# Optimization experiments

Hardware: AMD Instinct MI355X
Metric: run time of the kernel (lower is better)

Reference implementation:

```python
import jax, jax.numpy as jnp
import numpy as np

B, N, D = 16, 2048, 64

def setup_inputs() -> dict:
    key = jax.random.key(0)
    kq, kk, kv = jax.random.split(key, 3)
    queries = jax.random.normal(kq, (B, N, D), dtype=jnp.float32)
    keys = jax.random.normal(kk, (B, N, D), dtype=jnp.float32)
    values = jax.random.normal(kv, (B, N, D), dtype=jnp.float32)
    scaling_factor = jnp.asarray(np.sqrt(D), dtype=jnp.float32)
    return {"queries": queries, "keys": keys, "values": values, "scaling_factor": scaling_factor}

def reference(queries, keys, values, scaling_factor):
    # scores: [B, N, N] = Q K^T / scale
    scores = jnp.einsum('bqd,bkd->bqk', queries, keys) / scaling_factor
    atn = jax.nn.softmax(scores, axis=2)
    return jnp.einsum('bqk,bkd->bqd', atn, values)
```

## Files before the change

kernel.cpp:

```cpp
#include <hip/hip_runtime.h>
#include <hip/hip_bf16.h>

#define BATCH 16
#define SEQ 2048
#define DIM 64

typedef __attribute__((ext_vector_type(8))) __bf16 bf16x8;
typedef __attribute__((ext_vector_type(8))) unsigned short u16x8;
typedef __attribute__((ext_vector_type(2))) unsigned int u32x2;
typedef __attribute__((ext_vector_type(4))) unsigned int u32x4;
typedef __attribute__((ext_vector_type(16))) float f32x16;

#if __has_builtin(__builtin_amdgcn_exp2f)
#define EXP2F(x) __builtin_amdgcn_exp2f(x)
#else
#define EXP2F(x) __expf(0.69314718055994531f * (x))
#endif

__device__ __forceinline__ unsigned short f2bf_hw(float f) {
    __bf16 h = (__bf16)f;
    return __builtin_bit_cast(unsigned short, h);
}

__device__ __forceinline__ unsigned int pk_bf16(float lo, float hi) {
    unsigned int a = f2bf_hw(lo), b = f2bf_hw(hi);
    return a | (b << 16);
}

__device__ __forceinline__ void half_swap(unsigned int a, unsigned int b,
                                          unsigned int& lo, unsigned int& hi) {
#if __has_builtin(__builtin_amdgcn_permlane32_swap)
    u32x2 r = __builtin_amdgcn_permlane32_swap(a, b, false, false);
    lo = r[0];
    hi = r[1];
#else
    unsigned int sa = (unsigned int)__shfl_xor((int)a, 32);
    unsigned int sb = (unsigned int)__shfl_xor((int)b, 32);
    const bool hh = (threadIdx.x & 32) != 0;
    lo = hh ? sb : a;
    hi = hh ? b : sa;
#endif
}

__global__ __launch_bounds__(256)
void preconvert_kv(const float* __restrict__ K, const float* __restrict__ V,
                   unsigned short* __restrict__ Ks, unsigned short* __restrict__ Vts) {
    __shared__ float vt[128 * 65];
    const int tid = threadIdx.x;
    const int x = blockIdx.x;
    const int b = ((x & 7) << 1) | ((x >> 3) & 1);
    const int kpath = (x >> 4) & 1;
    const int t = x >> 5;
    if (kpath) {
        const float* src = K + ((size_t)(b * SEQ + t * 128)) * DIM;
        unsigned short* dst = Ks + ((size_t)(b * 16 + t)) * 8192;
        #pragma unroll
        for (int p = 0; p < 4; ++p) {
            const int cid = p * 256 + tid;
            const int key = cid >> 3, g = cid & 7;
            const int d0 = (g >> 1) * 16 + (g & 1) * 8;
            float4 x0 = *(const float4*)(src + key * DIM + d0);
            float4 x1 = *(const float4*)(src + key * DIM + d0 + 4);
            u16x8 o;
            o[0] = f2bf_hw(x0.x); o[1] = f2bf_hw(x0.y); o[2] = f2bf_hw(x0.z); o[3] = f2bf_hw(x0.w);
            o[4] = f2bf_hw(x1.x); o[5] = f2bf_hw(x1.y); o[6] = f2bf_hw(x1.z); o[7] = f2bf_hw(x1.w);
            *(u16x8*)(dst + (g * 128 + key) * 8) = o;
        }
    } else {
        const float* src = V + ((size_t)(b * SEQ + t * 128)) * DIM;
        #pragma unroll
        for (int p = 0; p < 8; ++p) {
            const int f = p * 256 + tid;
            const int row = f >> 4, c4 = (f & 15) << 2;
            float4 xv = *(const float4*)(src + row * DIM + c4);
            vt[row * 65 + c4 + 0] = xv.x; vt[row * 65 + c4 + 1] = xv.y;
            vt[row * 65 + c4 + 2] = xv.z; vt[row * 65 + c4 + 3] = xv.w;
        }
        __syncthreads();
        unsigned short* dst = Vts + ((size_t)(b * 16 + t)) * 8192;
        #pragma unroll
        for (int p = 0; p < 4; ++p) {
            const int cid = p * 256 + tid;
            const int g = cid >> 6, d = cid & 63;
            const int k0 = (g >> 1) * 16 + (g & 1) * 8;
            u16x8 o;
            #pragma unroll
            for (int j = 0; j < 8; ++j) o[j] = f2bf_hw(vt[(k0 + j) * 65 + d]);
            *(u16x8*)(dst + (g * 64 + d) * 8) = o;
        }
    }
}

__global__ __launch_bounds__(256)
void attn_flash_kernel(const float* __restrict__ Q,
                       const unsigned short* __restrict__ Ks,
                       const unsigned short* __restrict__ Vts,
                       const float* __restrict__ scaling,
                       float* __restrict__ O) {
    __shared__ __attribute__((aligned(16))) unsigned short ring[3 * 4096];

    const int tid  = threadIdx.x;
    const int w    = tid >> 6;
    const int lane = tid & 63;
    const int m    = lane & 31;
    const int h    = lane >> 5;

    const int x  = blockIdx.x;
    const int b  = ((x & 7) << 1) | ((x >> 3) & 1);
    const int q0 = (x >> 4) * 128;

    const float csc = 1.4426950408889634f / scaling[0];

    bf16x8 aq[4];
    {
        const float* qsrc = Q + ((size_t)(b * SEQ + q0 + w * 32 + m)) * DIM + h * 8;
        #pragma unroll
        for (int c = 0; c < 4; ++c) {
            float4 x0 = *(const float4*)(qsrc + c * 16);
            float4 x1 = *(const float4*)(qsrc + c * 16 + 4);
            u32x4 pk;
            pk[0] = pk_bf16(x0.x * csc, x0.y * csc);
            pk[1] = pk_bf16(x0.z * csc, x0.w * csc);
            pk[2] = pk_bf16(x1.x * csc, x1.y * csc);
            pk[3] = pk_bf16(x1.z * csc, x1.w * csc);
            aq[c] = __builtin_bit_cast(bf16x8, pk);
        }
    }

    f32x16 Oacc[2];
    #pragma unroll
    for (int dt = 0; dt < 2; ++dt)
        #pragma unroll
        for (int r = 0; r < 16; ++r) Oacc[dt][r] = 0.f;
    float psum = 0.f;

    const unsigned short* Kb = Ks  + ((size_t)b * 16) * 8192;
    const unsigned short* Vb = Vts + ((size_t)b * 16) * 8192;
    const int qq = 2 * w + h;

    auto ld_k_g = [&](int s) -> u16x8 {
        const int it = s >> 2, tt = s & 3;
        return *(const u16x8*)(Kb + (size_t)it * 8192 +
                               (size_t)((qq * 128 + tt * 32 + m)) * 8);
    };
    auto ld_v_g = [&](int s) -> u16x8 {
        const int it = s >> 2, tt = s & 3;
        return *(const u16x8*)(Vb + (size_t)it * 8192 +
                               (size_t)((((2 * tt + (qq >> 2)) * 2 + ((qq >> 1) & 1)) * 64 +
                                         (qq & 1) * 32 + m)) * 8);
    };
    auto st_lds = [&](int slot, u16x8 kv, u16x8 vv) {
        *(u16x8*)(&ring[slot * 4096 + w * 512 + lane * 8]) = kv;
        *(u16x8*)(&ring[slot * 4096 + 2048 + w * 512 + lane * 8]) = vv;
    };
    auto ld_kc = [&](int slot, bf16x8* kc) {
        #pragma unroll
        for (int c = 0; c < 4; ++c)
            kc[c] = __builtin_bit_cast(bf16x8,
                *(const u16x8*)(&ring[slot * 4096 + (c * 2 + h) * 256 + m * 8]));
    };
    auto ld_bv = [&](int slot, bf16x8 (*bv)[2]) {
        #pragma unroll
        for (int c2 = 0; c2 < 2; ++c2)
            #pragma unroll
            for (int dt = 0; dt < 2; ++dt)
                bv[c2][dt] = __builtin_bit_cast(bf16x8,
                    *(const u16x8*)(&ring[slot * 4096 + 2048 +
                                          (c2 * 4 + h * 2 + dt) * 256 + m * 8]));
    };
    auto calc_s = [&](const bf16x8* kc, f32x16& S) {
        #pragma unroll
        for (int r = 0; r < 16; ++r) S[r] = 0.f;
        #pragma unroll
        for (int c = 0; c < 4; ++c)
            S = __builtin_amdgcn_mfma_f32_32x32x16_bf16(kc[c], aq[c], S, 0, 0, 0);
    };
    auto exp_swap = [&](const f32x16& S, bf16x8* pbo) {
        unsigned int d0[8];
        #pragma unroll
        for (int k = 0; k < 4; ++k) {
            float a0 = EXP2F(S[4 * k + 0]), a1 = EXP2F(S[4 * k + 1]);
            float a2 = EXP2F(S[4 * k + 2]), a3 = EXP2F(S[4 * k + 3]);
            psum += (a0 + a1) + (a2 + a3);
            d0[2 * k + 0] = pk_bf16(a0, a1);
            d0[2 * k + 1] = pk_bf16(a2, a3);
        }
        #pragma unroll
        for (int c2 = 0; c2 < 2; ++c2) {
            u32x4 bw;
            unsigned int lo, hi;
            half_swap(d0[4 * c2 + 0], d0[4 * c2 + 2], lo, hi);
            bw[0] = lo; bw[2] = hi;
            half_swap(d0[4 * c2 + 1], d0[4 * c2 + 3], lo, hi);
            bw[1] = lo; bw[3] = hi;
            pbo[c2] = __builtin_bit_cast(bf16x8, bw);
        }
    };
    auto pv = [&](bf16x8 (*bv)[2], bf16x8* pb) {
        #pragma unroll
        for (int c2 = 0; c2 < 2; ++c2)
            #pragma unroll
            for (int dt = 0; dt < 2; ++dt)
                Oacc[dt] = __builtin_amdgcn_mfma_f32_32x32x16_bf16(bv[c2][dt], pb[c2], Oacc[dt], 0, 0, 0);
    };

    u16x8 rgK = ld_k_g(0), rgV = ld_v_g(0);
    u16x8 nK  = ld_k_g(1), nV  = ld_v_g(1);
    st_lds(0, rgK, rgV);
    rgK = nK; rgV = nV;
    asm volatile("s_waitcnt lgkmcnt(0)" ::: "memory");
    __builtin_amdgcn_sched_barrier(0);
    __builtin_amdgcn_s_barrier();
    __builtin_amdgcn_sched_barrier(0);

    bf16x8 bvH[2][2];
    bf16x8 pbH[2];
    {
        const u32x4 z = {0u, 0u, 0u, 0u};
        #pragma unroll
        for (int c2 = 0; c2 < 2; ++c2) {
            pbH[c2] = __builtin_bit_cast(bf16x8, z);
            #pragma unroll
            for (int dt = 0; dt < 2; ++dt) bvH[c2][dt] = __builtin_bit_cast(bf16x8, z);
        }
    }

    int sl = 0;
    #pragma unroll 1
    for (int t = 0; t < 63; ++t) {
        const int s2 = (t + 2 < 64) ? t + 2 : 63;
        u16x8 aK = ld_k_g(s2), aV = ld_v_g(s2);

        pv(bvH, pbH);

        bf16x8 kc[4];
        ld_kc(sl, kc);
        f32x16 S;
        calc_s(kc, S);
        ld_bv(sl, bvH);
        exp_swap(S, pbH);

        const int wslot = (sl == 2) ? 0 : sl + 1;
        st_lds(wslot, rgK, rgV);
        rgK = aK; rgV = aV;

        asm volatile("s_waitcnt lgkmcnt(0)" ::: "memory");
        __builtin_amdgcn_sched_barrier(0);
        __builtin_amdgcn_s_barrier();
        __builtin_amdgcn_sched_barrier(0);
        sl = wslot;
    }

    {
        pv(bvH, pbH);
        bf16x8 kc[4];
        ld_kc(sl, kc);
        f32x16 S;
        calc_s(kc, S);
        ld_bv(sl, bvH);
        exp_swap(S, pbH);
        pv(bvH, pbH);
    }

    float l = psum + __shfl_xor(psum, 32);
    const float invl = 1.0f / l;
    float* orow = O + ((size_t)(b * SEQ + q0 + w * 32 + m)) * DIM;
    #pragma unroll
    for (int dt = 0; dt < 2; ++dt) {
        #pragma unroll
        for (int k = 0; k < 4; ++k) {
            float4 o4;
            #pragma unroll
            for (int j = 0; j < 4; ++j)
                ((float*)&o4)[j] = Oacc[dt][4 * k + j] * invl;
            *(float4*)(orow + dt * 32 + 8 * k + 4 * h) = o4;
        }
    }
}

extern "C" void kernel_launch(void* const* d_in, const int* in_sizes, int n_in,
                              void* d_out, int out_size, void* d_ws, size_t ws_size,
                              hipStream_t stream) {
    const float* Q = (const float*)d_in[0];
    const float* K = (const float*)d_in[1];
    const float* V = (const float*)d_in[2];
    const float* scaling = (const float*)d_in[3];
    float* O = (float*)d_out;

    unsigned short* Ks  = (unsigned short*)d_ws;
    unsigned short* Vts = Ks + (size_t)BATCH * 16 * 8192;

    preconvert_kv<<<dim3(512), dim3(256), 0, stream>>>(K, V, Ks, Vts);
    attn_flash_kernel<<<dim3(256), dim3(256), 0, stream>>>(Q, Ks, Vts, scaling, O);
}
```

Baseline: 112.5 us.

## Split key range across wave pairs and halve query tile to double grid

The attention kernel now processes 64 queries per block instead of 128. Each pair of waves handles half of the key sequence with its own LDS ring, and the two partial outputs and row sums are merged through LDS at the end. The grid doubles to 512 blocks, which fills more CUs on a 256-CU part. The software-pipelined loop is simplified: PV runs in the same iteration, s_setprio is added, and 2-block occupancy is requested. The preconvert kernel is likewise split into half-tiles to double its grid. In exchange, each block re-reads K/V per block pair, so global traffic grows, and the merge adds a reduction step and a barrier.

```diff
diff --git a/kernel.cpp b/kernel.cpp
--- a/kernel.cpp
+++ b/kernel.cpp
@@ -45,19 +45,20 @@
 __global__ __launch_bounds__(256)
 void preconvert_kv(const float* __restrict__ K, const float* __restrict__ V,
                    unsigned short* __restrict__ Ks, unsigned short* __restrict__ Vts) {
-    __shared__ float vt[128 * 65];
+    __shared__ float vt[64 * 65];
     const int tid = threadIdx.x;
     const int x = blockIdx.x;
     const int b = ((x & 7) << 1) | ((x >> 3) & 1);
     const int kpath = (x >> 4) & 1;
-    const int t = x >> 5;
+    const int t = (x >> 5) & 15;
+    const int half = (x >> 9) & 1;
     if (kpath) {
         const float* src = K + ((size_t)(b * SEQ + t * 128)) * DIM;
         unsigned short* dst = Ks + ((size_t)(b * 16 + t)) * 8192;
         #pragma unroll
-        for (int p = 0; p < 4; ++p) {
+        for (int p = 0; p < 2; ++p) {
             const int cid = p * 256 + tid;
-            const int key = cid >> 3, g = cid & 7;
+            const int key = half * 64 + (cid >> 3), g = cid & 7;
             const int d0 = (g >> 1) * 16 + (g & 1) * 8;
             float4 x0 = *(const float4*)(src + key * DIM + d0);
             float4 x1 = *(const float4*)(src + key * DIM + d0 + 4);
@@ -67,9 +68,9 @@
             *(u16x8*)(dst + (g * 128 + key) * 8) = o;
         }
     } else {
-        const float* src = V + ((size_t)(b * SEQ + t * 128)) * DIM;
-        #pragma unroll
-        for (int p = 0; p < 8; ++p) {
+        const float* src = V + ((size_t)(b * SEQ + t * 128 + half * 64)) * DIM;
+        #pragma unroll
+        for (int p = 0; p < 4; ++p) {
             const int f = p * 256 + tid;
             const int row = f >> 4, c4 = (f & 15) << 2;
             float4 xv = *(const float4*)(src + row * DIM + c4);
@@ -79,10 +80,11 @@
         __syncthreads();
         unsigned short* dst = Vts + ((size_t)(b * 16 + t)) * 8192;
         #pragma unroll
-        for (int p = 0; p < 4; ++p) {
+        for (int p = 0; p < 2; ++p) {
             const int cid = p * 256 + tid;
-            const int g = cid >> 6, d = cid & 63;
-            const int k0 = (g >> 1) * 16 + (g & 1) * 8;
+            const int gl = cid >> 6, d = cid & 63;
+            const int g = half * 8 + gl;
+            const int k0 = (g >> 1) * 16 + (g & 1) * 8 - half * 64;
             u16x8 o;
             #pragma unroll
             for (int j = 0; j < 8; ++j) o[j] = f2bf_hw(vt[(k0 + j) * 65 + d]);
@@ -91,29 +93,31 @@
     }
 }
 
-__global__ __launch_bounds__(256)
+__global__ __launch_bounds__(256, 2)
 void attn_flash_kernel(const float* __restrict__ Q,
                        const unsigned short* __restrict__ Ks,
                        const unsigned short* __restrict__ Vts,
                        const float* __restrict__ scaling,
                        float* __restrict__ O) {
-    __shared__ __attribute__((aligned(16))) unsigned short ring[3 * 4096];
+    __shared__ __attribute__((aligned(16))) unsigned short ring[2][3][4096];
 
     const int tid  = threadIdx.x;
     const int w    = tid >> 6;
     const int lane = tid & 63;
     const int m    = lane & 31;
     const int h    = lane >> 5;
+    const int kh   = w >> 1;
+    const int qs   = w & 1;
 
     const int x  = blockIdx.x;
     const int b  = ((x & 7) << 1) | ((x >> 3) & 1);
-    const int q0 = (x >> 4) * 128;
+    const int q0 = (x >> 4) * 64;
 
     const float csc = 1.4426950408889634f / scaling[0];
 
     bf16x8 aq[4];
     {
-        const float* qsrc = Q + ((size_t)(b * SEQ + q0 + w * 32 + m)) * DIM + h * 8;
+        const float* qsrc = Q + ((size_t)(b * SEQ + q0 + qs * 32 + m)) * DIM + h * 8;
         #pragma unroll
         for (int c = 0; c < 4; ++c) {
             float4 x0 = *(const float4*)(qsrc + c * 16);
@@ -134,30 +138,38 @@
         for (int r = 0; r < 16; ++r) Oacc[dt][r] = 0.f;
     float psum = 0.f;
 
-    const unsigned short* Kb = Ks  + ((size_t)b * 16) * 8192;
-    const unsigned short* Vb = Vts + ((size_t)b * 16) * 8192;
-    const int qq = 2 * w + h;
-
-    auto ld_k_g = [&](int s) -> u16x8 {
+    const unsigned short* Kbh = Ks  + ((size_t)(b * 16 + kh * 8)) * 8192;
+    const unsigned short* Vbh = Vts + ((size_t)(b * 16 + kh * 8)) * 8192;
+
+    const int L  = qs * 64 + lane;
+    const int i0 = 2 * L, i1 = 2 * L + 1;
+    const int g0 = i0 >> 5, mk0 = i0 & 31;
+    const int g1 = i1 >> 5, mk1 = i1 & 31;
+    const int c20 = g0 >> 2, hh0 = (g0 >> 1) & 1, dd0 = g0 & 1;
+    const int c21 = g1 >> 2, hh1 = (g1 >> 1) & 1, dd1 = g1 & 1;
+
+    u16x8 rk0, rk1, rv0, rv1;
+    auto load_sub = [&](int s) {
         const int it = s >> 2, tt = s & 3;
-        return *(const u16x8*)(Kb + (size_t)it * 8192 +
-                               (size_t)((qq * 128 + tt * 32 + m)) * 8);
-    };
-    auto ld_v_g = [&](int s) -> u16x8 {
-        const int it = s >> 2, tt = s & 3;
-        return *(const u16x8*)(Vb + (size_t)it * 8192 +
-                               (size_t)((((2 * tt + (qq >> 2)) * 2 + ((qq >> 1) & 1)) * 64 +
-                                         (qq & 1) * 32 + m)) * 8);
-    };
-    auto st_lds = [&](int slot, u16x8 kv, u16x8 vv) {
-        *(u16x8*)(&ring[slot * 4096 + w * 512 + lane * 8]) = kv;
-        *(u16x8*)(&ring[slot * 4096 + 2048 + w * 512 + lane * 8]) = vv;
+        const unsigned short* Kt = Kbh + (size_t)it * 8192;
+        const unsigned short* Vt = Vbh + (size_t)it * 8192;
+        rk0 = *(const u16x8*)(Kt + (g0 * 128 + tt * 32 + mk0) * 8);
+        rk1 = *(const u16x8*)(Kt + (g1 * 128 + tt * 32 + mk1) * 8);
+        rv0 = *(const u16x8*)(Vt + (((2 * tt + c20) * 2 + hh0) * 64 + dd0 * 32 + mk0) * 8);
+        rv1 = *(const u16x8*)(Vt + (((2 * tt + c21) * 2 + hh1) * 64 + dd1 * 32 + mk1) * 8);
+    };
+    auto st_sub = [&](int slot) {
+        unsigned short* base = &ring[kh][slot][0];
+        *(u16x8*)(base + i0 * 8) = rk0;
+        *(u16x8*)(base + i1 * 8) = rk1;
+        *(u16x8*)(base + 2048 + i0 * 8) = rv0;
+        *(u16x8*)(base + 2048 + i1 * 8) = rv1;
     };
     auto ld_kc = [&](int slot, bf16x8* kc) {
         #pragma unroll
         for (int c = 0; c < 4; ++c)
             kc[c] = __builtin_bit_cast(bf16x8,
-                *(const u16x8*)(&ring[slot * 4096 + (c * 2 + h) * 256 + m * 8]));
+                *(const u16x8*)(&ring[kh][slot][((c * 2 + h) * 32 + m) * 8]));
     };
     auto ld_bv = [&](int slot, bf16x8 (*bv)[2]) {
         #pragma unroll
@@ -165,17 +177,35 @@
             #pragma unroll
             for (int dt = 0; dt < 2; ++dt)
                 bv[c2][dt] = __builtin_bit_cast(bf16x8,
-                    *(const u16x8*)(&ring[slot * 4096 + 2048 +
-                                          (c2 * 4 + h * 2 + dt) * 256 + m * 8]));
-    };
-    auto calc_s = [&](const bf16x8* kc, f32x16& S) {
+                    *(const u16x8*)(&ring[kh][slot][2048 + ((c2 * 4 + h * 2 + dt) * 32 + m) * 8]));
+    };
+    auto barrier_phase = [&]() {
+        asm volatile("s_waitcnt lgkmcnt(0)" ::: "memory");
+        __builtin_amdgcn_sched_barrier(0);
+        __builtin_amdgcn_s_barrier();
+        __builtin_amdgcn_sched_barrier(0);
+    };
+
+    load_sub(0); st_sub(0);
+    load_sub(1); st_sub(1);
+    load_sub(2);
+    barrier_phase();
+
+    int sl = 0, ws = 2;
+    #pragma unroll 1
+    for (int t = 0; t < 32; ++t) {
+        bf16x8 kc[4];
+        ld_kc(sl, kc);
+        f32x16 S;
         #pragma unroll
         for (int r = 0; r < 16; ++r) S[r] = 0.f;
         #pragma unroll
         for (int c = 0; c < 4; ++c)
             S = __builtin_amdgcn_mfma_f32_32x32x16_bf16(kc[c], aq[c], S, 0, 0, 0);
-    };
-    auto exp_swap = [&](const f32x16& S, bf16x8* pbo) {
+
+        bf16x8 bv[2][2];
+        ld_bv(sl, bv);
+
         unsigned int d0[8];
         #pragma unroll
         for (int k = 0; k < 4; ++k) {
@@ -185,6 +215,7 @@
             d0[2 * k + 0] = pk_bf16(a0, a1);
             d0[2 * k + 1] = pk_bf16(a2, a3);
         }
+        bf16x8 pb[2];
         #pragma unroll
         for (int c2 = 0; c2 < 2; ++c2) {
             u32x4 bw;
@@ -193,87 +224,53 @@
             bw[0] = lo; bw[2] = hi;
             half_swap(d0[4 * c2 + 1], d0[4 * c2 + 3], lo, hi);
             bw[1] = lo; bw[3] = hi;
-            pbo[c2] = __builtin_bit_cast(bf16x8, bw);
-        }
-    };
-    auto pv = [&](bf16x8 (*bv)[2], bf16x8* pb) {
+            pb[c2] = __builtin_bit_cast(bf16x8, bw);
+        }
+        __builtin_amdgcn_s_setprio(1);
         #pragma unroll
         for (int c2 = 0; c2 < 2; ++c2)
             #pragma unroll
             for (int dt = 0; dt < 2; ++dt)
                 Oacc[dt] = __builtin_amdgcn_mfma_f32_32x32x16_bf16(bv[c2][dt], pb[c2], Oacc[dt], 0, 0, 0);
-    };
-
-    u16x8 rgK = ld_k_g(0), rgV = ld_v_g(0);
-    u16x8 nK  = ld_k_g(1), nV  = ld_v_g(1);
-    st_lds(0, rgK, rgV);
-    rgK = nK; rgV = nV;
-    asm volatile("s_waitcnt lgkmcnt(0)" ::: "memory");
-    __builtin_amdgcn_sched_barrier(0);
-    __builtin_amdgcn_s_barrier();
-    __builtin_amdgcn_sched_barrier(0);
-
-    bf16x8 bvH[2][2];
-    bf16x8 pbH[2];
-    {
-        const u32x4 z = {0u, 0u, 0u, 0u};
-        #pragma unroll
-        for (int c2 = 0; c2 < 2; ++c2) {
-            pbH[c2] = __builtin_bit_cast(bf16x8, z);
-            #pragma unroll
-            for (int dt = 0; dt < 2; ++dt) bvH[c2][dt] = __builtin_bit_cast(bf16x8, z);
-        }
-    }
-
-    int sl = 0;
-    #pragma unroll 1
-    for (int t = 0; t < 63; ++t) {
-        const int s2 = (t + 2 < 64) ? t + 2 : 63;
-        u16x8 aK = ld_k_g(s2), aV = ld_v_g(s2);
-
-        pv(bvH, pbH);
-
-        bf16x8 kc[4];
-        ld_kc(sl, kc);
-        f32x16 S;
-        calc_s(kc, S);
-        ld_bv(sl, bvH);
-        exp_swap(S, pbH);
-
-        const int wslot = (sl == 2) ? 0 : sl + 1;
-        st_lds(wslot, rgK, rgV);
-        rgK = aK; rgV = aV;
-
-        asm volatile("s_waitcnt lgkmcnt(0)" ::: "memory");
-        __builtin_amdgcn_sched_barrier(0);
-        __builtin_amdgcn_s_barrier();
-        __builtin_amdgcn_sched_barrier(0);
-        sl = wslot;
-    }
-
-    {
-        pv(bvH, pbH);
-        bf16x8 kc[4];
-        ld_kc(sl, kc);
-        f32x16 S;
-        calc_s(kc, S);
-        ld_bv(sl, bvH);
-        exp_swap(S, pbH);
-        pv(bvH, pbH);
+        __builtin_amdgcn_s_setprio(0);
+
+        st_sub(ws);
+        const int s3 = (t + 3 < 32) ? t + 3 : 31;
+        load_sub(s3);
+        barrier_phase();
+
+        sl = (sl == 2) ? 0 : sl + 1;
+        ws = (ws == 2) ? 0 : ws + 1;
     }
 
     float l = psum + __shfl_xor(psum, 32);
-    const float invl = 1.0f / l;
-    float* orow = O + ((size_t)(b * SEQ + q0 + w * 32 + m)) * DIM;
-    #pragma unroll
-    for (int dt = 0; dt < 2; ++dt) {
-        #pragma unroll
-        for (int k = 0; k < 4; ++k) {
-            float4 o4;
-            #pragma unroll
-            for (int j = 0; j < 4; ++j)
-                ((float*)&o4)[j] = Oacc[dt][4 * k + j] * invl;
-            *(float4*)(orow + dt * 32 + 8 * k + 4 * h) = o4;
+    float* C = (float*)&ring[0][0][0];
+    if (kh == 1) {
+        float* dst = C + (qs * 64 + lane) * 33;
+        #pragma unroll
+        for (int dt = 0; dt < 2; ++dt)
+            #pragma unroll
+            for (int r = 0; r < 16; ++r)
+                dst[dt * 16 + r] = Oacc[dt][r];
+        dst[32] = l;
+    }
+    __syncthreads();
+    if (kh == 0) {
+        const float* src = C + (qs * 64 + lane) * 33;
+        const float invl = 1.0f / (l + src[32]);
+        float* orow = O + ((size_t)(b * SEQ + q0 + qs * 32 + m)) * DIM;
+        #pragma unroll
+        for (int dt = 0; dt < 2; ++dt) {
+            #pragma unroll
+            for (int k = 0; k < 4; ++k) {
+                float4 o4;
+                #pragma unroll
+                for (int j = 0; j < 4; ++j) {
+                    const int r = 4 * k + j;
+                    ((float*)&o4)[j] = (Oacc[dt][r] + src[dt * 16 + r]) * invl;
+                }
+                *(float4*)(orow + dt * 32 + 8 * k + 4 * h) = o4;
+            }
         }
     }
 }
@@ -290,6 +287,6 @@
     unsigned short* Ks  = (unsigned short*)d_ws;
     unsigned short* Vts = Ks + (size_t)BATCH * 16 * 8192;
 
-    preconvert_kv<<<dim3(512), dim3(256), 0, stream>>>(K, V, Ks, Vts);
-    attn_flash_kernel<<<dim3(256), dim3(256), 0, stream>>>(Q, Ks, Vts, scaling, O);
-}
+    preconvert_kv<<<dim3(1024), dim3(256), 0, stream>>>(K, V, Ks, Vts);
+    attn_flash_kernel<<<dim3(BATCH * (SEQ / 64)), dim3(256), 0, stream>>>(Q, Ks, Vts, scaling, O);
+}
```

After: 104.1 us. -7.5%, faster.
